# Optimization experiments

Hardware: AMD Instinct MI355X
Metric: run time of the kernel (lower is better)

The kernel has to match this reference:

```python
import jax, jax.numpy as jnp
import numpy as np

N, E, F_IN, HID, HEADS, OUT = 50000, 800000, 128, 64, 4, 40


def gat_layer(x, src, dst, n, W, a_src, a_dst, b, heads, ch):
    # PyG GATConv: h = x @ W per head; e_ij = LeakyReLU(a_src.h_j + a_dst.h_i)
    h = (x @ W).reshape(n, heads, ch)
    al_s = jnp.einsum('nhc,hc->nh', h, a_src)  # source-side logit term
    al_d = jnp.einsum('nhc,hc->nh', h, a_dst)  # target-side logit term
    e = jax.nn.leaky_relu(al_s[src] + al_d[dst], negative_slope=0.2)  # [E,H]
    m = jax.ops.segment_max(e, dst, num_segments=n)  # stable softmax per target node
    e = jnp.exp(e - m[dst])
    s = jax.ops.segment_sum(e, dst, num_segments=n)
    alpha = e / s[dst]  # [E,H]
    out = jax.ops.segment_sum(h[src] * alpha[:, :, None], dst, num_segments=n)  # [n,H,C]
    return out.reshape(n, heads * ch) + b


def gat_forward(x, src, dst, W0, as0, ad0, b0, W1, as1, ad1, b1, W2, as2, ad2, b2):
    n = x.shape[0]
    x = jax.nn.elu(gat_layer(x, src, dst, n, W0, as0, ad0, b0, HEADS, HID))
    x = jax.nn.elu(gat_layer(x, src, dst, n, W1, as1, ad1, b1, HEADS, HID))
    x = gat_layer(x, src, dst, n, W2, as2, ad2, b2, 1, OUT)
    return jax.nn.log_softmax(x, axis=1)


def setup_inputs() -> dict:
    key = jax.random.key(0)
    ks = jax.random.split(key, 16)
    x = jax.random.normal(ks[0], (N, F_IN), dtype=jnp.float32)
    edge_index = jax.random.randint(ks[1], (2, E), 0, N, dtype=jnp.int64)
    g = lambda k, sh: jax.random.normal(k, sh, dtype=jnp.float32) * (1.0 / np.sqrt(sh[0]))
    d_hid = HID * HEADS
    return {
        'x': x, 'edge_index': edge_index,
        'W0': g(ks[2], (F_IN, d_hid)), 'as0': g(ks[3], (HEADS, HID)), 'ad0': g(ks[4], (HEADS, HID)), 'b0': jnp.zeros((d_hid,), jnp.float32),
        'W1': g(ks[5], (d_hid, d_hid)), 'as1': g(ks[6], (HEADS, HID)), 'ad1': g(ks[7], (HEADS, HID)), 'b1': jnp.zeros((d_hid,), jnp.float32),
        'W2': g(ks[8], (d_hid, OUT)), 'as2': g(ks[9], (1, OUT)), 'ad2': g(ks[10], (1, OUT)), 'b2': jnp.zeros((OUT,), jnp.float32),
    }


def reference(x, edge_index, W0, as0, ad0, b0, W1, as1, ad1, b1, W2, as2, ad2, b2):
    n = x.shape[0]
    loops = jnp.arange(n, dtype=edge_index.dtype)  # PyG add_self_loops=True
    src = jnp.concatenate([edge_index[0], loops])
    dst = jnp.concatenate([edge_index[1], loops])
    return gat_forward(x, src, dst, W0, as0, ad0, b0, W1, as1, ad1, b1, W2, as2, ad2, b2)
```

## Files before the change

kernel.cpp:

```cpp
#include <hip/hip_runtime.h>
#include <math.h>

#define NODES 50000
#define NEDGES 800000
#define TOT_E (NEDGES + NODES)
#define SCAN_B 256
#define SCAN_NB ((NODES + SCAN_B - 1) / SCAN_B)

typedef __attribute__((ext_vector_type(8))) short short8v;
typedef __attribute__((ext_vector_type(4))) float f32x4;

static __device__ __forceinline__ float lrelu(float z) {
  return z > 0.f ? z : 0.2f * z;
}
static __device__ __forceinline__ float b2f(ushort u) {
  union { uint i; float f; } v; v.i = ((uint)u) << 16; return v.f;
}
static __device__ __forceinline__ ushort f2b(float f) {
  union { float f; uint i; } v; v.f = f;
  uint r = v.i + 0x7fff + ((v.i >> 16) & 1);
  return (ushort)(r >> 16);
}

__global__ void k_hist(const int* __restrict__ dst, int* __restrict__ counts) {
  int stride = gridDim.x * blockDim.x;
  for (int i = blockIdx.x * blockDim.x + threadIdx.x; i < TOT_E; i += stride) {
    int d = (i < NEDGES) ? dst[i] : (i - NEDGES);
    atomicAdd(&counts[d], 1);
  }
}

__global__ __launch_bounds__(SCAN_B) void k_scan_red(const int* __restrict__ counts,
                                                     int* __restrict__ bsum) {
  __shared__ int sm[SCAN_B];
  int idx = blockIdx.x * SCAN_B + threadIdx.x;
  int v = (idx < NODES) ? counts[idx] : 0;
  sm[threadIdx.x] = v;
  __syncthreads();
  for (int off = SCAN_B / 2; off > 0; off >>= 1) {
    if (threadIdx.x < off) sm[threadIdx.x] += sm[threadIdx.x + off];
    __syncthreads();
  }
  if (threadIdx.x == 0) bsum[blockIdx.x] = sm[0];
}

__global__ __launch_bounds__(256) void k_scan_part(const int* __restrict__ bsum,
                                                   int* __restrict__ bpre) {
  __shared__ int sm[256];
  int tid = threadIdx.x;
  int v = (tid < SCAN_NB) ? bsum[tid] : 0;
  sm[tid] = v;
  __syncthreads();
  for (int off = 1; off < 256; off <<= 1) {
    int t = (tid >= off) ? sm[tid - off] : 0;
    __syncthreads();
    sm[tid] += t;
    __syncthreads();
  }
  if (tid < SCAN_NB) bpre[tid] = sm[tid] - v;
}

__global__ __launch_bounds__(SCAN_B) void k_scan_emit(const int* __restrict__ counts,
    const int* __restrict__ bpre, int* __restrict__ offs, int* __restrict__ cur) {
  __shared__ int sm[SCAN_B];
  int idx = blockIdx.x * SCAN_B + threadIdx.x;
  int tid = threadIdx.x;
  int v = (idx < NODES) ? counts[idx] : 0;
  sm[tid] = v;
  __syncthreads();
  for (int off = 1; off < SCAN_B; off <<= 1) {
    int t = (tid >= off) ? sm[tid - off] : 0;
    __syncthreads();
    sm[tid] += t;
    __syncthreads();
  }
  int base = bpre[blockIdx.x];
  int excl = base + sm[tid] - v;
  if (idx < NODES) { offs[idx] = excl; cur[idx] = excl; }
  if (idx == NODES - 1) offs[NODES] = excl + v;
}

__global__ void k_scatter(const int* __restrict__ src, const int* __restrict__ dst,
                          int* __restrict__ cur, int* __restrict__ ssrc) {
  int stride = gridDim.x * blockDim.x;
  for (int i = blockIdx.x * blockDim.x + threadIdx.x; i < TOT_E; i += stride) {
    int s, d;
    if (i < NEDGES) { s = src[i]; d = dst[i]; } else { s = i - NEDGES; d = s; }
    int pos = atomicAdd(&cur[d], 1);
    ssrc[pos] = s;
  }
}

__global__ void k_cast4(const float* __restrict__ X, ushort* __restrict__ Xb, int total4) {
  int stride = gridDim.x * blockDim.x;
  for (int i = blockIdx.x * blockDim.x + threadIdx.x; i < total4; i += stride) {
    float4 v = *(const float4*)&X[i * 4];
    ushort4 o;
    o.x = f2b(v.x); o.y = f2b(v.y); o.z = f2b(v.z); o.w = f2b(v.w);
    *(ushort4*)&Xb[i * 4] = o;
  }
}

__global__ void k_packB(const float* __restrict__ W, ushort* __restrict__ Bp,
                        int N, int NF, int total) {
  int idx = blockIdx.x * blockDim.x + threadIdx.x;
  if (idx >= total) return;
  int i = idx & 7;
  int lane = (idx >> 3) & 63;
  int rem = idx >> 9;
  int nf = rem % NF;
  int kf = rem / NF;
  int k = kf * 32 + (lane >> 4) * 8 + i;
  int col = nf * 16 + (lane & 15);
  float v = (col < N) ? W[(size_t)k * N + col] : 0.f;
  Bp[idx] = f2b(v);
}

template<int KF, int NFW, int CG, int HEADS, int NF_TOT>
__global__ __launch_bounds__(256, 2) void k_gemm_reg(
    const ushort* __restrict__ A, const ushort* __restrict__ Bp,
    ushort* __restrict__ H, const float* __restrict__ a_s, const float* __restrict__ a_d,
    float* __restrict__ al_s, float* __restrict__ al_d, int M, int N, int K) {
  int wave = (blockIdx.x * blockDim.x + threadIdx.x) >> 6;
  int lane = threadIdx.x & 63;
  int lg = lane >> 4;
  int lr = lane & 15;
  int total_waves = (gridDim.x * blockDim.x) >> 6;
  int wpc = total_waves / CG;
  int cg = wave / wpc;
  int mslot = wave - cg * wpc;
  if (cg >= CG) return;

  short8v b[KF][NFW];
#pragma unroll
  for (int kf = 0; kf < KF; ++kf)
#pragma unroll
    for (int n = 0; n < NFW; ++n)
      b[kf][n] = *(const short8v*)(Bp + ((size_t)(kf * NF_TOT + cg * NFW + n) * 64 + lane) * 8);

  float asc[NFW], adc[NFW];
#pragma unroll
  for (int n = 0; n < NFW; ++n) {
    int col = (cg * NFW + n) * 16 + lr;
    bool ok = col < N;
    asc[n] = ok ? a_s[col] : 0.f;
    adc[n] = ok ? a_d[col] : 0.f;
  }

  int nstrips = M >> 4;
  for (int strip = mslot; strip < nstrips; strip += wpc) {
    const ushort* arow = A + (size_t)(strip * 16 + lr) * K + lg * 8;
    short8v a[KF];
#pragma unroll
    for (int kf = 0; kf < KF; ++kf) a[kf] = *(const short8v*)(arow + kf * 32);
    f32x4 acc[NFW];
#pragma unroll
    for (int n = 0; n < NFW; ++n) acc[n] = (f32x4){0.f, 0.f, 0.f, 0.f};
#pragma unroll
    for (int kf = 0; kf < KF; ++kf)
#pragma unroll
      for (int n = 0; n < NFW; ++n)
        acc[n] = __builtin_amdgcn_mfma_f32_16x16x32_bf16(a[kf], b[kf][n], acc[n], 0, 0, 0);

#pragma unroll
    for (int n = 0; n < NFW; ++n) {
      int col = (cg * NFW + n) * 16 + lr;
      if (col < N) {
#pragma unroll
        for (int r = 0; r < 4; ++r) {
          int row = strip * 16 + lg * 4 + r;
          H[(size_t)row * N + col] = f2b(acc[n][r]);
        }
      }
    }

    float ps[4], pd[4];
#pragma unroll
    for (int r = 0; r < 4; ++r) {
      float s = 0.f, d = 0.f;
#pragma unroll
      for (int n = 0; n < NFW; ++n) {
        s += acc[n][r] * asc[n];
        d += acc[n][r] * adc[n];
      }
      ps[r] = s; pd[r] = d;
    }
#pragma unroll
    for (int off = 1; off <= 8; off <<= 1)
#pragma unroll
      for (int t = 0; t < 4; ++t) {
        ps[t] += __shfl_xor(ps[t], off);
        pd[t] += __shfl_xor(pd[t], off);
      }
    if (lr < 4) {
      int row = strip * 16 + lg * 4 + lr;
      if (HEADS == 4) {
        al_s[row * 4 + cg] = ps[lr];
        al_d[row * 4 + cg] = pd[lr];
      } else {
        al_s[row] = ps[lr];
        al_d[row] = pd[lr];
      }
    }
  }
}

__global__ __launch_bounds__(256) void k_agg4(const ushort* __restrict__ hb,
    const float* __restrict__ al_s, const float* __restrict__ al_d,
    const int* __restrict__ offs, const int* __restrict__ ssrc,
    const float* __restrict__ bias, ushort* __restrict__ outb) {
  int wid = (blockIdx.x * blockDim.x + threadIdx.x) >> 6;
  if (wid >= NODES) return;
  int lane = threadIdx.x & 63;
  int beg = offs[wid], end = offs[wid + 1];
  int h1 = lane >> 4;
  int es = lane & 15;
  float ald = al_d[wid * 4 + h1];

  float m = -1e30f, s = 0.f;
  for (int i = beg + es; i < end; i += 16) {
    int sv = ssrc[i];
    float z = lrelu(al_s[sv * 4 + h1] + ald);
    if (z > m) { s = s * __expf(m - z) + 1.f; m = z; }
    else s += __expf(z - m);
  }
#pragma unroll
  for (int off = 1; off <= 8; off <<= 1) {
    float mo = __shfl_xor(m, off), so = __shfl_xor(s, off);
    float mn = fmaxf(m, mo);
    s = s * __expf(m - mn) + so * __expf(mo - mn);
    m = mn;
  }
  float inv = 1.f / s;

  int half = lane >> 5;
  int cl = lane & 31;
  int hh = cl >> 3;
  int srcl = hh * 16;
  float mh = __shfl(m, srcl);
  float invh = __shfl(inv, srcl);
  float aldh = __shfl(ald, srcl);
  float acc[8] = {0.f, 0.f, 0.f, 0.f, 0.f, 0.f, 0.f, 0.f};
  int i = beg + half;
  for (; i + 2 < end; i += 4) {
    int sv0 = ssrc[i], sv1 = ssrc[i + 2];
    float z0 = lrelu(al_s[sv0 * 4 + hh] + aldh);
    float z1 = lrelu(al_s[sv1 * 4 + hh] + aldh);
    float a0 = __expf(z0 - mh) * invh;
    float a1 = __expf(z1 - mh) * invh;
    short8v hv0 = *(const short8v*)(hb + (size_t)sv0 * 256 + cl * 8);
    short8v hv1 = *(const short8v*)(hb + (size_t)sv1 * 256 + cl * 8);
#pragma unroll
    for (int j = 0; j < 8; ++j) acc[j] += a0 * b2f((ushort)hv0[j]);
#pragma unroll
    for (int j = 0; j < 8; ++j) acc[j] += a1 * b2f((ushort)hv1[j]);
  }
  for (; i < end; i += 2) {
    int sv = ssrc[i];
    float z = lrelu(al_s[sv * 4 + hh] + aldh);
    float alpha = __expf(z - mh) * invh;
    short8v hv = *(const short8v*)(hb + (size_t)sv * 256 + cl * 8);
#pragma unroll
    for (int j = 0; j < 8; ++j) acc[j] += alpha * b2f((ushort)hv[j]);
  }
#pragma unroll
  for (int j = 0; j < 8; ++j) acc[j] += __shfl_xor(acc[j], 32);
  if (half == 0) {
    short8v o;
#pragma unroll
    for (int j = 0; j < 8; ++j) {
      float v = acc[j] + bias[cl * 8 + j];
      o[j] = (short)f2b(v > 0.f ? v : __expf(v) - 1.f);
    }
    *(short8v*)(outb + (size_t)wid * 256 + cl * 8) = o;
  }
}

__global__ __launch_bounds__(256) void k_agg1(const ushort* __restrict__ hb,
    const float* __restrict__ al_s, const float* __restrict__ al_d,
    const int* __restrict__ offs, const int* __restrict__ ssrc,
    const float* __restrict__ bias, float* __restrict__ out) {
  int wid = (blockIdx.x * blockDim.x + threadIdx.x) >> 6;
  if (wid >= NODES) return;
  int lane = threadIdx.x & 63;
  int beg = offs[wid], end = offs[wid + 1];
  float ald = al_d[wid];

  float m = -1e30f, s = 0.f;
  for (int i = beg + lane; i < end; i += 64) {
    float z = lrelu(al_s[ssrc[i]] + ald);
    if (z > m) { s = s * __expf(m - z) + 1.f; m = z; }
    else s += __expf(z - m);
  }
#pragma unroll
  for (int off = 1; off <= 32; off <<= 1) {
    float mo = __shfl_xor(m, off), so = __shfl_xor(s, off);
    float mn = fmaxf(m, mo);
    s = s * __expf(m - mn) + so * __expf(mo - mn);
    m = mn;
  }
  float inv = 1.f / s;

  int e = lane >> 4;
  int q = lane & 15;
  bool act = q < 10;
  float acc[4] = {0.f, 0.f, 0.f, 0.f};
  int i = beg + e;
  for (; i + 4 < end; i += 8) {
    int sv0 = ssrc[i], sv1 = ssrc[i + 4];
    float z0 = lrelu(al_s[sv0] + ald);
    float z1 = lrelu(al_s[sv1] + ald);
    float a0 = __expf(z0 - m) * inv;
    float a1 = __expf(z1 - m) * inv;
    if (act) {
      ushort4 hv0 = *(const ushort4*)&hb[(size_t)sv0 * 40 + q * 4];
      ushort4 hv1 = *(const ushort4*)&hb[(size_t)sv1 * 40 + q * 4];
      acc[0] += a0 * b2f(hv0.x) + a1 * b2f(hv1.x);
      acc[1] += a0 * b2f(hv0.y) + a1 * b2f(hv1.y);
      acc[2] += a0 * b2f(hv0.z) + a1 * b2f(hv1.z);
      acc[3] += a0 * b2f(hv0.w) + a1 * b2f(hv1.w);
    }
  }
  for (; i < end; i += 4) {
    int sv = ssrc[i];
    float z = lrelu(al_s[sv] + ald);
    float alpha = __expf(z - m) * inv;
    if (act) {
      ushort4 hv = *(const ushort4*)&hb[(size_t)sv * 40 + q * 4];
      acc[0] += alpha * b2f(hv.x); acc[1] += alpha * b2f(hv.y);
      acc[2] += alpha * b2f(hv.z); acc[3] += alpha * b2f(hv.w);
    }
  }
#pragma unroll
  for (int j = 0; j < 4; ++j) {
    acc[j] += __shfl_xor(acc[j], 16);
    acc[j] += __shfl_xor(acc[j], 32);
  }
  float v[4];
  float mm = -1e30f;
  if (act) {
#pragma unroll
    for (int j = 0; j < 4; ++j) {
      v[j] = acc[j] + bias[q * 4 + j];
      mm = fmaxf(mm, v[j]);
    }
  }
#pragma unroll
  for (int off = 1; off <= 8; off <<= 1) mm = fmaxf(mm, __shfl_xor(mm, off));
  float se = 0.f;
  if (act) {
#pragma unroll
    for (int j = 0; j < 4; ++j) se += __expf(v[j] - mm);
  }
#pragma unroll
  for (int off = 1; off <= 8; off <<= 1) se += __shfl_xor(se, off);
  if (act && e == 0) {
    float lse = mm + __logf(se);
    float4 o;
    o.x = v[0] - lse; o.y = v[1] - lse; o.z = v[2] - lse; o.w = v[3] - lse;
    *(float4*)&out[(size_t)wid * 40 + q * 4] = o;
  }
}

extern "C" void kernel_launch(void* const* d_in, const int* in_sizes, int n_in,
                              void* d_out, int out_size, void* d_ws, size_t ws_size,
                              hipStream_t stream) {
  const float* x   = (const float*)d_in[0];
  const int*   ei  = (const int*)d_in[1];
  const float* W0  = (const float*)d_in[2];
  const float* as0 = (const float*)d_in[3];
  const float* ad0 = (const float*)d_in[4];
  const float* b0  = (const float*)d_in[5];
  const float* W1  = (const float*)d_in[6];
  const float* as1 = (const float*)d_in[7];
  const float* ad1 = (const float*)d_in[8];
  const float* b1  = (const float*)d_in[9];
  const float* W2  = (const float*)d_in[10];
  const float* as2 = (const float*)d_in[11];
  const float* ad2 = (const float*)d_in[12];
  const float* b2  = (const float*)d_in[13];
  float* out = (float*)d_out;

  char* p = (char*)d_ws;
  auto take = [&](size_t bytes) {
    char* q = p;
    p += (bytes + 255) & ~(size_t)255;
    return (void*)q;
  };
  ushort* xb0 = (ushort*)take((size_t)NODES * 128 * 2);
  ushort* xb1 = (ushort*)take((size_t)NODES * 256 * 2);
  ushort* xb2 = (ushort*)take((size_t)NODES * 256 * 2);
  ushort* hb  = (ushort*)take((size_t)NODES * 256 * 2);
  float* als  = (float*)take((size_t)NODES * 4 * 4);
  float* ald  = (float*)take((size_t)NODES * 4 * 4);
  int* ssrc   = (int*)take((size_t)TOT_E * 4);
  int* offs   = (int*)take((size_t)(NODES + 1) * 4);
  int* cur    = (int*)take((size_t)NODES * 4);
  int* cnt    = (int*)take((size_t)NODES * 4);
  int* bsum   = (int*)take((size_t)SCAN_NB * 4);
  int* bpre   = (int*)take((size_t)SCAN_NB * 4);
  ushort* Bp0 = (ushort*)take((size_t)4 * 16 * 512 * 2);
  ushort* Bp1 = (ushort*)take((size_t)8 * 16 * 512 * 2);
  ushort* Bp2 = (ushort*)take((size_t)8 * 3 * 512 * 2);

  hipMemsetAsync(cnt, 0, (size_t)NODES * 4, stream);
  k_hist<<<2048, 256, 0, stream>>>(ei + NEDGES, cnt);
  k_scan_red<<<SCAN_NB, SCAN_B, 0, stream>>>(cnt, bsum);
  k_scan_part<<<1, 256, 0, stream>>>(bsum, bpre);
  k_scan_emit<<<SCAN_NB, SCAN_B, 0, stream>>>(cnt, bpre, offs, cur);
  k_scatter<<<2048, 256, 0, stream>>>(ei, ei + NEDGES, cur, ssrc);

  k_cast4<<<2048, 256, 0, stream>>>(x, xb0, NODES * 128 / 4);
  {
    int t0 = 4 * 16 * 512;  k_packB<<<(t0 + 255) / 256, 256, 0, stream>>>(W0, Bp0, 256, 16, t0);
    int t1 = 8 * 16 * 512;  k_packB<<<(t1 + 255) / 256, 256, 0, stream>>>(W1, Bp1, 256, 16, t1);
    int t2 = 8 * 3 * 512;   k_packB<<<(t2 + 255) / 256, 256, 0, stream>>>(W2, Bp2, 40, 3, t2);
  }

  int nwb = (NODES * 64 + 255) / 256;
  int ggb = 512;

  k_gemm_reg<4, 4, 4, 4, 16><<<ggb, 256, 0, stream>>>(xb0, Bp0, hb, as0, ad0, als, ald, NODES, 256, 128);
  k_agg4<<<nwb, 256, 0, stream>>>(hb, als, ald, offs, ssrc, b0, xb1);

  k_gemm_reg<8, 4, 4, 4, 16><<<ggb, 256, 0, stream>>>(xb1, Bp1, hb, as1, ad1, als, ald, NODES, 256, 256);
  k_agg4<<<nwb, 256, 0, stream>>>(hb, als, ald, offs, ssrc, b1, xb2);

  k_gemm_reg<8, 3, 1, 1, 3><<<ggb, 256, 0, stream>>>(xb2, Bp2, hb, as2, ad2, als, ald, NODES, 40, 256);
  k_agg1<<<nwb, 256, 0, stream>>>(hb, als, ald, offs, ssrc, b2, out);
}
```

Baseline: 337.2 us.

## Compute edge attention once per chunk and broadcast via shuffles in aggregation

New measurement: 356.0 us. 5.6% more time.

```diff
diff --git a/kernel.cpp b/kernel.cpp
--- a/kernel.cpp
+++ b/kernel.cpp
@@ -213,66 +213,89 @@
   if (wid >= NODES) return;
   int lane = threadIdx.x & 63;
   int beg = offs[wid], end = offs[wid + 1];
-  int h1 = lane >> 4;
-  int es = lane & 15;
-  float ald = al_d[wid * 4 + h1];
-
-  float m = -1e30f, s = 0.f;
-  for (int i = beg + es; i < end; i += 16) {
+  float4 ald4 = *(const float4*)&al_d[wid * 4];
+
+  float m[4], s[4];
+#pragma unroll
+  for (int h = 0; h < 4; ++h) { m[h] = -1e30f; s[h] = 0.f; }
+  for (int i = beg + lane; i < end; i += 64) {
     int sv = ssrc[i];
-    float z = lrelu(al_s[sv * 4 + h1] + ald);
-    if (z > m) { s = s * __expf(m - z) + 1.f; m = z; }
-    else s += __expf(z - m);
-  }
-#pragma unroll
-  for (int off = 1; off <= 8; off <<= 1) {
-    float mo = __shfl_xor(m, off), so = __shfl_xor(s, off);
-    float mn = fmaxf(m, mo);
-    s = s * __expf(m - mn) + so * __expf(mo - mn);
-    m = mn;
-  }
-  float inv = 1.f / s;
-
-  int half = lane >> 5;
-  int cl = lane & 31;
-  int hh = cl >> 3;
-  int srcl = hh * 16;
-  float mh = __shfl(m, srcl);
-  float invh = __shfl(inv, srcl);
-  float aldh = __shfl(ald, srcl);
-  float acc[8] = {0.f, 0.f, 0.f, 0.f, 0.f, 0.f, 0.f, 0.f};
-  int i = beg + half;
-  for (; i + 2 < end; i += 4) {
-    int sv0 = ssrc[i], sv1 = ssrc[i + 2];
-    float z0 = lrelu(al_s[sv0 * 4 + hh] + aldh);
-    float z1 = lrelu(al_s[sv1 * 4 + hh] + aldh);
-    float a0 = __expf(z0 - mh) * invh;
-    float a1 = __expf(z1 - mh) * invh;
-    short8v hv0 = *(const short8v*)(hb + (size_t)sv0 * 256 + cl * 8);
-    short8v hv1 = *(const short8v*)(hb + (size_t)sv1 * 256 + cl * 8);
-#pragma unroll
-    for (int j = 0; j < 8; ++j) acc[j] += a0 * b2f((ushort)hv0[j]);
-#pragma unroll
-    for (int j = 0; j < 8; ++j) acc[j] += a1 * b2f((ushort)hv1[j]);
-  }
-  for (; i < end; i += 2) {
-    int sv = ssrc[i];
-    float z = lrelu(al_s[sv * 4 + hh] + aldh);
-    float alpha = __expf(z - mh) * invh;
-    short8v hv = *(const short8v*)(hb + (size_t)sv * 256 + cl * 8);
-#pragma unroll
-    for (int j = 0; j < 8; ++j) acc[j] += alpha * b2f((ushort)hv[j]);
-  }
-#pragma unroll
-  for (int j = 0; j < 8; ++j) acc[j] += __shfl_xor(acc[j], 32);
-  if (half == 0) {
-    short8v o;
+    float4 a4 = *(const float4*)&al_s[sv * 4];
+    float z0 = lrelu(a4.x + ald4.x), z1 = lrelu(a4.y + ald4.y);
+    float z2 = lrelu(a4.z + ald4.z), z3 = lrelu(a4.w + ald4.w);
+    float z[4] = {z0, z1, z2, z3};
+#pragma unroll
+    for (int h = 0; h < 4; ++h) {
+      if (z[h] > m[h]) { s[h] = s[h] * __expf(m[h] - z[h]) + 1.f; m[h] = z[h]; }
+      else s[h] += __expf(z[h] - m[h]);
+    }
+  }
+#pragma unroll
+  for (int off = 1; off <= 32; off <<= 1) {
+#pragma unroll
+    for (int h = 0; h < 4; ++h) {
+      float mo = __shfl_xor(m[h], off), so = __shfl_xor(s[h], off);
+      float mn = fmaxf(m[h], mo);
+      s[h] = s[h] * __expf(m[h] - mn) + so * __expf(mo - mn);
+      m[h] = mn;
+    }
+  }
+  float inv[4];
+#pragma unroll
+  for (int h = 0; h < 4; ++h) inv[h] = 1.f / s[h];
+
+  int q = lane >> 4;
+  int c = lane & 15;
+  int hsel = c >> 2;
+  float facc[16];
+#pragma unroll
+  for (int j = 0; j < 16; ++j) facc[j] = 0.f;
+
+  for (int cb = beg; cb < end; cb += 64) {
+    int cnt = min(64, end - cb);
+    float av0 = 0.f, av1 = 0.f, av2 = 0.f, av3 = 0.f;
+    int myidx = 0;
+    if (lane < cnt) {
+      myidx = ssrc[cb + lane];
+      float4 a4 = *(const float4*)&al_s[myidx * 4];
+      av0 = __expf(lrelu(a4.x + ald4.x) - m[0]) * inv[0];
+      av1 = __expf(lrelu(a4.y + ald4.y) - m[1]) * inv[1];
+      av2 = __expf(lrelu(a4.z + ald4.z) - m[2]) * inv[2];
+      av3 = __expf(lrelu(a4.w + ald4.w) - m[3]) * inv[3];
+    }
+    for (int e = 0; e < cnt; e += 4) {
+      int eq = e + q;
+      int sv = __shfl(myidx, eq);
+      float a0 = __shfl(av0, eq), a1 = __shfl(av1, eq);
+      float a2 = __shfl(av2, eq), a3 = __shfl(av3, eq);
+      float al = hsel == 0 ? a0 : (hsel == 1 ? a1 : (hsel == 2 ? a2 : a3));
+      if (eq < cnt) {
+        const ushort* hr = hb + (size_t)sv * 256 + c * 16;
+        short8v v0 = *(const short8v*)hr;
+        short8v v1 = *(const short8v*)(hr + 8);
+#pragma unroll
+        for (int j = 0; j < 8; ++j) facc[j] += al * b2f((ushort)v0[j]);
+#pragma unroll
+        for (int j = 0; j < 8; ++j) facc[j + 8] += al * b2f((ushort)v1[j]);
+      }
+    }
+  }
+#pragma unroll
+  for (int j = 0; j < 16; ++j) {
+    facc[j] += __shfl_xor(facc[j], 16);
+    facc[j] += __shfl_xor(facc[j], 32);
+  }
+  if (q == 0) {
+    short8v o0, o1;
 #pragma unroll
     for (int j = 0; j < 8; ++j) {
-      float v = acc[j] + bias[cl * 8 + j];
-      o[j] = (short)f2b(v > 0.f ? v : __expf(v) - 1.f);
-    }
-    *(short8v*)(outb + (size_t)wid * 256 + cl * 8) = o;
+      float v = facc[j] + bias[c * 16 + j];
+      o0[j] = (short)f2b(v > 0.f ? v : __expf(v) - 1.f);
+      float w = facc[j + 8] + bias[c * 16 + 8 + j];
+      o1[j] = (short)f2b(w > 0.f ? w : __expf(w) - 1.f);
+    }
+    *(short8v*)(outb + (size_t)wid * 256 + c * 16) = o0;
+    *(short8v*)(outb + (size_t)wid * 256 + c * 16 + 8) = o1;
   }
 }
 
@@ -301,34 +324,27 @@
   }
   float inv = 1.f / s;
 
-  int e = lane >> 4;
-  int q = lane & 15;
-  bool act = q < 10;
+  int q = lane >> 4;
+  int cq = lane & 15;
+  bool act = cq < 10;
   float acc[4] = {0.f, 0.f, 0.f, 0.f};
-  int i = beg + e;
-  for (; i + 4 < end; i += 8) {
-    int sv0 = ssrc[i], sv1 = ssrc[i + 4];
-    float z0 = lrelu(al_s[sv0] + ald);
-    float z1 = lrelu(al_s[sv1] + ald);
-    float a0 = __expf(z0 - m) * inv;
-    float a1 = __expf(z1 - m) * inv;
-    if (act) {
-      ushort4 hv0 = *(const ushort4*)&hb[(size_t)sv0 * 40 + q * 4];
-      ushort4 hv1 = *(const ushort4*)&hb[(size_t)sv1 * 40 + q * 4];
-      acc[0] += a0 * b2f(hv0.x) + a1 * b2f(hv1.x);
-      acc[1] += a0 * b2f(hv0.y) + a1 * b2f(hv1.y);
-      acc[2] += a0 * b2f(hv0.z) + a1 * b2f(hv1.z);
-      acc[3] += a0 * b2f(hv0.w) + a1 * b2f(hv1.w);
-    }
-  }
-  for (; i < end; i += 4) {
-    int sv = ssrc[i];
-    float z = lrelu(al_s[sv] + ald);
-    float alpha = __expf(z - m) * inv;
-    if (act) {
-      ushort4 hv = *(const ushort4*)&hb[(size_t)sv * 40 + q * 4];
-      acc[0] += alpha * b2f(hv.x); acc[1] += alpha * b2f(hv.y);
-      acc[2] += alpha * b2f(hv.z); acc[3] += alpha * b2f(hv.w);
+  for (int cb = beg; cb < end; cb += 64) {
+    int cnt = min(64, end - cb);
+    float av = 0.f;
+    int myidx = 0;
+    if (lane < cnt) {
+      myidx = ssrc[cb + lane];
+      av = __expf(lrelu(al_s[myidx] + ald) - m) * inv;
+    }
+    for (int e = 0; e < cnt; e += 4) {
+      int eq = e + q;
+      int sv = __shfl(myidx, eq);
+      float al = __shfl(av, eq);
+      if (eq < cnt && act) {
+        ushort4 hv = *(const ushort4*)&hb[(size_t)sv * 40 + cq * 4];
+        acc[0] += al * b2f(hv.x); acc[1] += al * b2f(hv.y);
+        acc[2] += al * b2f(hv.z); acc[3] += al * b2f(hv.w);
+      }
     }
   }
 #pragma unroll
@@ -341,7 +357,7 @@
   if (act) {
 #pragma unroll
     for (int j = 0; j < 4; ++j) {
-      v[j] = acc[j] + bias[q * 4 + j];
+      v[j] = acc[j] + bias[cq * 4 + j];
       mm = fmaxf(mm, v[j]);
     }
   }
@@ -354,11 +370,11 @@
   }
 #pragma unroll
   for (int off = 1; off <= 8; off <<= 1) se += __shfl_xor(se, off);
-  if (act && e == 0) {
+  if (act && q == 0) {
     float lse = mm + __logf(se);
     float4 o;
     o.x = v[0] - lse; o.y = v[1] - lse; o.z = v[2] - lse; o.w = v[3] - lse;
-    *(float4*)&out[(size_t)wid * 40 + q * 4] = o;
+    *(float4*)&out[(size_t)wid * 40 + cq * 4] = o;
   }
 }
 
```
